# Kernel tuning notes

Hardware: AMD Instinct MI355X
Metric: run time of the kernel (lower is better)

## Reference

```python
import jax, jax.numpy as jnp
import numpy as np

D_K = 64
NEG_INF = -1.0e9


def setup_inputs() -> dict:
    key = jax.random.key(0)
    kq, kk, kv = jax.random.split(key, 3)
    B, H, S, D = 2, 16, 2048, D_K
    Q = jax.random.normal(kq, (B, H, S, D), dtype=jnp.float32)
    K = jax.random.normal(kk, (B, H, S, D), dtype=jnp.float32)
    V = jax.random.normal(kv, (B, H, S, D), dtype=jnp.float32)
    # causal mask: True where attention is DISALLOWED (strict upper triangle)
    attn_mask = jnp.triu(jnp.ones((S, S), dtype=bool), k=1)
    return {"Q": Q, "K": K, "V": V, "attn_mask": attn_mask}


def reference(Q, K, V, attn_mask):
    # scores = Q @ (K / sqrt(d_k))^T  -> [B,H,S,S]
    scale = 1.0 / np.sqrt(D_K).astype(np.float32)
    scores = jnp.einsum("bhqd,bhkd->bhqk", Q, K * scale)
    scores = jnp.where(attn_mask, NEG_INF, scores)  # masked_fill_(mask, -1e9)
    attn = jax.nn.softmax(scores, axis=-1)
    context = jnp.einsum("bhqk,bhkd->bhqd", attn, V)
    return (context, attn)
```

## Files before the change

### kernel.cpp

```cpp
#include <hip/hip_runtime.h>

constexpr int S_LEN = 2048;
constexpr int D_K   = 64;
constexpr int N_BH  = 32;
constexpr int KB    = 64;

typedef __attribute__((ext_vector_type(8))) short short8;
typedef __attribute__((ext_vector_type(4))) float f32x4;
typedef unsigned short ushort_t;

__device__ __forceinline__ unsigned short f2bf(float f) {
    unsigned int u = __builtin_bit_cast(unsigned int, f);
    u += 0x7fffu + ((u >> 16) & 1u);
    return (unsigned short)(u >> 16);
}
__device__ __forceinline__ float bf2f(unsigned short h) {
    unsigned int u = ((unsigned int)h) << 16;
    return __builtin_bit_cast(float, u);
}

__global__ __launch_bounds__(256)
void prep_k(const float* __restrict__ K, ushort_t* __restrict__ Kws) {
    const int idx = blockIdx.x * 256 + threadIdx.x;
    const float4* src = (const float4*)K + (size_t)idx * 2;
    float4 a = src[0], b = src[1];
    float x[8] = {a.x, a.y, a.z, a.w, b.x, b.y, b.z, b.w};
    short8 o;
    #pragma unroll
    for (int j = 0; j < 8; ++j) o[j] = (short)f2bf(x[j] * 0.125f);
    *(short8*)(Kws + (size_t)idx * 8) = o;
}

__global__ __launch_bounds__(256)
void prep_v(const float* __restrict__ V, ushort_t* __restrict__ Vws) {
    const int gid = blockIdx.x * 256 + threadIdx.x;
    const int u   = gid & 511;
    const int bc  = gid >> 9;
    const int c   = bc & 31;
    const int bh  = bc >> 5;
    const int kg  = u >> 6;
    const int d   = u & 63;
    const float* vp = V + ((size_t)bh * S_LEN + c * KB + kg * 8) * D_K + d;
    short8 o;
    #pragma unroll
    for (int i = 0; i < 8; ++i) o[i] = (short)f2bf(vp[(size_t)i * D_K]);
    *(short8*)(Vws + ((size_t)(bh * 32 + c) * D_K + d) * KB + kg * 8) = o;
}

__global__ __launch_bounds__(256, 4)
void sdpa_main(const float* __restrict__ Q, const ushort_t* __restrict__ Kws,
               const ushort_t* __restrict__ Vws, float* __restrict__ out)
{
    __shared__ __align__(16) ushort_t Kbuf[2][4096];
    __shared__ __align__(16) ushort_t Vbuf[2][4096];
    __shared__ __align__(16) ushort_t Plds[4][1024];

    const int tid = threadIdx.x;
    const int w   = tid >> 6;
    const int l   = tid & 63;
    const int lr  = l & 15;
    const int lh  = l >> 4;

    const int bx  = blockIdx.x;
    const int g   = bx >> 8;
    const int idx = bx & 255;
    const int bh  = idx >> 3;
    const int r   = idx & 7;
    int t;
    switch (g) {
        case 0:  t = r;      break;
        case 1:  t = 15 - r; break;
        case 2:  t = 16 + r; break;
        default: t = 31 - r; break;
    }
    const int nch = t + 1;
    const int q0  = t * 64;
    const int qg_base = q0 + w * 16 + lh * 4;

    float* ctx_out  = out;
    float* attn_out = out + (size_t)N_BH * S_LEN * D_K;

    const short8* Kt  = (const short8*)(Kws + (size_t)bh * S_LEN * D_K);
    const short8* Vt8 = (const short8*)(Vws + (size_t)bh * 32 * 4096);

    const int wrow0  = tid >> 3;
    const int wcol   = (tid & 7) << 4;
    const int wphys0 = wrow0 * 128 + (wcol ^ ((wrow0 & 7) << 4));
    const int wphys1 = wphys0 + 32 * 128;
    const int rsw    = (lr & 7) << 4;

    short8 qhi[2], qlo[2];
    {
        const float* qrow = Q + ((size_t)bh * S_LEN + q0 + w * 16 + lr) * D_K;
        #pragma unroll
        for (int ds = 0; ds < 2; ++ds) {
            const float4* p4 = (const float4*)(qrow + ds * 32 + lh * 8);
            float4 a = p4[0], bq = p4[1];
            float x[8] = {a.x, a.y, a.z, a.w, bq.x, bq.y, bq.z, bq.w};
            short8 hi, lo;
            #pragma unroll
            for (int j = 0; j < 8; ++j) {
                unsigned short h = f2bf(x[j]);
                hi[j] = (short)h;
                lo[j] = (short)f2bf(x[j] - bf2f(h));
            }
            qhi[ds] = hi; qlo[ds] = lo;
        }
    }

    float inv_[4];
    {
        float sum[4] = {0.f, 0.f, 0.f, 0.f};

        auto p1 = [&](const char* Kb, int c) {
            #pragma unroll
            for (int nt = 0; nt < 4; ++nt) {
                f32x4 acc = {0.f, 0.f, 0.f, 0.f};
                #pragma unroll
                for (int ks = 0; ks < 2; ++ks) {
                    short8 bk = *(const short8*)(Kb + (nt * 16 + lr) * 128 + ((ks * 64 + lh * 16) ^ rsw));
                    acc = __builtin_amdgcn_mfma_f32_16x16x32_bf16(qhi[ks], bk, acc, 0, 0, 0);
                }
                const int kg = c * KB + nt * 16 + lr;
                #pragma unroll
                for (int rr = 0; rr < 4; ++rr)
                    if (kg <= qg_base + rr) sum[rr] += __expf(fminf(acc[rr], 60.f));
            }
        };

        short8 kE0 = Kt[tid], kE1 = Kt[tid + 256];
        *(short8*)((char*)&Kbuf[0][0] + wphys0) = kE0;
        *(short8*)((char*)&Kbuf[0][0] + wphys1) = kE1;
        short8 kO0 = Kt[512 + tid], kO1 = Kt[512 + tid + 256];
        __syncthreads();
        for (int c = 0; c < nch; c += 2) {
            if (c + 2 < nch) { kE0 = Kt[(c + 2) * 512 + tid]; kE1 = Kt[(c + 2) * 512 + tid + 256]; }
            p1((const char*)&Kbuf[0][0], c);
            if (c + 1 < nch) {
                *(short8*)((char*)&Kbuf[1][0] + wphys0) = kO0;
                *(short8*)((char*)&Kbuf[1][0] + wphys1) = kO1;
            }
            __syncthreads();
            if (c + 1 < nch) {
                if (c + 3 < nch) { kO0 = Kt[(c + 3) * 512 + tid]; kO1 = Kt[(c + 3) * 512 + tid + 256]; }
                p1((const char*)&Kbuf[1][0], c + 1);
                if (c + 2 < nch) {
                    *(short8*)((char*)&Kbuf[0][0] + wphys0) = kE0;
                    *(short8*)((char*)&Kbuf[0][0] + wphys1) = kE1;
                }
                __syncthreads();
            }
        }
        #pragma unroll
        for (int rr = 0; rr < 4; ++rr) {
            float s = sum[rr];
            s += __shfl_xor(s, 1);
            s += __shfl_xor(s, 2);
            s += __shfl_xor(s, 4);
            s += __shfl_xor(s, 8);
            inv_[rr] = 1.f / s;
        }
    }

    f32x4 ctx[4];
    #pragma unroll
    for (int nt = 0; nt < 4; ++nt) ctx[nt] = (f32x4){0.f, 0.f, 0.f, 0.f};

    {
        auto p2 = [&](const char* Kb, const char* Vb, int c) {
            #pragma unroll
            for (int nt = 0; nt < 4; ++nt) {
                f32x4 acc = {0.f, 0.f, 0.f, 0.f};
                #pragma unroll
                for (int ks = 0; ks < 2; ++ks) {
                    short8 bk = *(const short8*)(Kb + (nt * 16 + lr) * 128 + ((ks * 64 + lh * 16) ^ rsw));
                    acc = __builtin_amdgcn_mfma_f32_16x16x32_bf16(qhi[ks], bk, acc, 0, 0, 0);
                    acc = __builtin_amdgcn_mfma_f32_16x16x32_bf16(qlo[ks], bk, acc, 0, 0, 0);
                }
                const int kg = c * KB + nt * 16 + lr;
                #pragma unroll
                for (int rr = 0; rr < 4; ++rr) {
                    const int pwr = lh * 4 + rr;
                    const int qg  = qg_base + rr;
                    float p = (kg <= qg) ? __expf(fminf(acc[rr], 60.f)) * inv_[rr] : 0.f;
                    attn_out[((size_t)bh * S_LEN + qg) * S_LEN + kg] = p;
                    Plds[w][pwr * 64 + ((nt * 16 + lr) ^ ((pwr & 7) << 3))] = f2bf(p);
                }
            }
            #pragma unroll
            for (int ks = 0; ks < 2; ++ks) {
                short8 pa = *(const short8*)&Plds[w][lr * 64 + ((ks * 32 + lh * 8) ^ ((lr & 7) << 3))];
                #pragma unroll
                for (int nt = 0; nt < 4; ++nt) {
                    short8 vb = *(const short8*)(Vb + (nt * 16 + lr) * 128 + ((ks * 64 + lh * 16) ^ rsw));
                    ctx[nt] = __builtin_amdgcn_mfma_f32_16x16x32_bf16(pa, vb, ctx[nt], 0, 0, 0);
                }
            }
        };

        short8 kE0 = Kt[tid],        kE1 = Kt[tid + 256];
        short8 vE0 = Vt8[tid],       vE1 = Vt8[tid + 256];
        *(short8*)((char*)&Kbuf[0][0] + wphys0) = kE0;
        *(short8*)((char*)&Kbuf[0][0] + wphys1) = kE1;
        *(short8*)((char*)&Vbuf[0][0] + wphys0) = vE0;
        *(short8*)((char*)&Vbuf[0][0] + wphys1) = vE1;
        short8 kO0 = Kt[512 + tid],  kO1 = Kt[512 + tid + 256];
        short8 vO0 = Vt8[512 + tid], vO1 = Vt8[512 + tid + 256];
        __syncthreads();
        for (int c = 0; c < nch; c += 2) {
            if (c + 2 < nch) {
                kE0 = Kt[(c + 2) * 512 + tid];  kE1 = Kt[(c + 2) * 512 + tid + 256];
                vE0 = Vt8[(c + 2) * 512 + tid]; vE1 = Vt8[(c + 2) * 512 + tid + 256];
            }
            p2((const char*)&Kbuf[0][0], (const char*)&Vbuf[0][0], c);
            if (c + 1 < nch) {
                *(short8*)((char*)&Kbuf[1][0] + wphys0) = kO0;
                *(short8*)((char*)&Kbuf[1][0] + wphys1) = kO1;
                *(short8*)((char*)&Vbuf[1][0] + wphys0) = vO0;
                *(short8*)((char*)&Vbuf[1][0] + wphys1) = vO1;
            }
            __syncthreads();
            if (c + 1 < nch) {
                if (c + 3 < nch) {
                    kO0 = Kt[(c + 3) * 512 + tid];  kO1 = Kt[(c + 3) * 512 + tid + 256];
                    vO0 = Vt8[(c + 3) * 512 + tid]; vO1 = Vt8[(c + 3) * 512 + tid + 256];
                }
                p2((const char*)&Kbuf[1][0], (const char*)&Vbuf[1][0], c + 1);
                if (c + 2 < nch) {
                    *(short8*)((char*)&Kbuf[0][0] + wphys0) = kE0;
                    *(short8*)((char*)&Kbuf[0][0] + wphys1) = kE1;
                    *(short8*)((char*)&Vbuf[0][0] + wphys0) = vE0;
                    *(short8*)((char*)&Vbuf[0][0] + wphys1) = vE1;
                }
                __syncthreads();
            }
        }
    }

    #pragma unroll
    for (int nt = 0; nt < 4; ++nt)
        #pragma unroll
        for (int rr = 0; rr < 4; ++rr)
            ctx_out[((size_t)bh * S_LEN + qg_base + rr) * D_K + nt * 16 + lr] = ctx[nt][rr];

    const int k0 = nch * KB;
    if (k0 < S_LEN) {
        const float4 z = {0.f, 0.f, 0.f, 0.f};
        float* rowp = attn_out + ((size_t)bh * S_LEN + q0 + (tid >> 2)) * S_LEN;
        for (int k = k0 + (tid & 3) * 4; k < S_LEN; k += 16)
            *(float4*)(rowp + k) = z;
    }
}

constexpr int LDP = 72;

__global__ __launch_bounds__(256)
void sdpa_fused_v1(const float* __restrict__ Q, const float* __restrict__ K,
                   const float* __restrict__ V, float* __restrict__ out)
{
    __shared__ __align__(16) unsigned short Klds[KB * LDP];
    __shared__ __align__(16) unsigned short Vtlds[D_K * LDP];
    __shared__ __align__(16) unsigned short Pl[4][16 * LDP];

    const int tid = threadIdx.x;
    const int w   = tid >> 6;
    const int l   = tid & 63;
    const int lr  = l & 15;
    const int lh  = l >> 4;

    const int bh   = blockIdx.y;
    const int qblk = (int)gridDim.x - 1 - (int)blockIdx.x;
    const int q0   = qblk * 64;
    const int qw   = q0 + w * 16;
    const int nchunks = qblk + 1;

    const size_t in_base = (size_t)bh * S_LEN * D_K;
    float* ctx_out  = out;
    float* attn_out = out + (size_t)N_BH * S_LEN * D_K;

    short8 qhi[2], qlo[2];
    {
        const float* qrow = Q + in_base + (size_t)(qw + lr) * D_K;
        #pragma unroll
        for (int ds = 0; ds < 2; ++ds) {
            const float4* p4 = (const float4*)(qrow + ds * 32 + lh * 8);
            float4 a = p4[0], b = p4[1];
            float x[8] = {a.x, a.y, a.z, a.w, b.x, b.y, b.z, b.w};
            short8 hi, lo;
            #pragma unroll
            for (int j = 0; j < 8; ++j) {
                unsigned short h = f2bf(x[j]);
                hi[j] = (short)h;
                lo[j] = (short)f2bf(x[j] - bf2f(h));
            }
            qhi[ds] = hi; qlo[ds] = lo;
        }
    }

    const int srow = tid >> 2;
    const int scol = (tid & 3) * 16;
    const float* kstage = K + in_base + (size_t)srow * D_K + scol;
    const float* vstage = V + in_base + (size_t)srow * D_K + scol;

    float inv_[4];
    {
        float sum[4] = {0.f, 0.f, 0.f, 0.f};
        for (int c = 0; c < nchunks; ++c) {
            {
                const float4* kp = (const float4*)(kstage + (size_t)c * KB * D_K);
                float4 a0 = kp[0], a1 = kp[1], a2 = kp[2], a3 = kp[3];
                float x[16] = {a0.x,a0.y,a0.z,a0.w, a1.x,a1.y,a1.z,a1.w,
                               a2.x,a2.y,a2.z,a2.w, a3.x,a3.y,a3.z,a3.w};
                short8 w0, w1;
                #pragma unroll
                for (int j = 0; j < 8; ++j) {
                    w0[j] = (short)f2bf(x[j]     * 0.125f);
                    w1[j] = (short)f2bf(x[j + 8] * 0.125f);
                }
                *(short8*)&Klds[srow * LDP + scol]     = w0;
                *(short8*)&Klds[srow * LDP + scol + 8] = w1;
            }
            __syncthreads();
            #pragma unroll
            for (int nt = 0; nt < 4; ++nt) {
                f32x4 acc = {0.f, 0.f, 0.f, 0.f};
                #pragma unroll
                for (int ks = 0; ks < 2; ++ks) {
                    short8 bk = *(const short8*)&Klds[(nt*16 + lr) * LDP + ks*32 + lh*8];
                    acc = __builtin_amdgcn_mfma_f32_16x16x32_bf16(qhi[ks], bk, acc, 0, 0, 0);
                    acc = __builtin_amdgcn_mfma_f32_16x16x32_bf16(qlo[ks], bk, acc, 0, 0, 0);
                }
                const int kg = c * KB + nt * 16 + lr;
                #pragma unroll
                for (int rr = 0; rr < 4; ++rr) {
                    if (kg <= qw + lh * 4 + rr)
                        sum[rr] += __expf(fminf(acc[rr], 60.f));
                }
            }
            __syncthreads();
        }
        #pragma unroll
        for (int rr = 0; rr < 4; ++rr) {
            float t = sum[rr];
            t += __shfl_xor(t, 1);
            t += __shfl_xor(t, 2);
            t += __shfl_xor(t, 4);
            t += __shfl_xor(t, 8);
            inv_[rr] = 1.f / t;
        }
    }

    f32x4 ctx[4];
    #pragma unroll
    for (int nt = 0; nt < 4; ++nt) ctx[nt] = (f32x4){0.f, 0.f, 0.f, 0.f};

    for (int c = 0; c < nchunks; ++c) {
        {
            const float4* kp = (const float4*)(kstage + (size_t)c * KB * D_K);
            float4 a0 = kp[0], a1 = kp[1], a2 = kp[2], a3 = kp[3];
            float x[16] = {a0.x,a0.y,a0.z,a0.w, a1.x,a1.y,a1.z,a1.w,
                           a2.x,a2.y,a2.z,a2.w, a3.x,a3.y,a3.z,a3.w};
            short8 w0, w1;
            #pragma unroll
            for (int j = 0; j < 8; ++j) {
                w0[j] = (short)f2bf(x[j]     * 0.125f);
                w1[j] = (short)f2bf(x[j + 8] * 0.125f);
            }
            *(short8*)&Klds[srow * LDP + scol]     = w0;
            *(short8*)&Klds[srow * LDP + scol + 8] = w1;

            const float4* vp = (const float4*)(vstage + (size_t)c * KB * D_K);
            float4 b0 = vp[0], b1 = vp[1], b2 = vp[2], b3 = vp[3];
            float y[16] = {b0.x,b0.y,b0.z,b0.w, b1.x,b1.y,b1.z,b1.w,
                           b2.x,b2.y,b2.z,b2.w, b3.x,b3.y,b3.z,b3.w};
            #pragma unroll
            for (int j = 0; j < 16; ++j)
                Vtlds[(scol + j) * LDP + srow] = f2bf(y[j]);
        }
        __syncthreads();

        #pragma unroll
        for (int nt = 0; nt < 4; ++nt) {
            f32x4 acc = {0.f, 0.f, 0.f, 0.f};
            #pragma unroll
            for (int ks = 0; ks < 2; ++ks) {
                short8 bk = *(const short8*)&Klds[(nt*16 + lr) * LDP + ks*32 + lh*8];
                acc = __builtin_amdgcn_mfma_f32_16x16x32_bf16(qhi[ks], bk, acc, 0, 0, 0);
                acc = __builtin_amdgcn_mfma_f32_16x16x32_bf16(qlo[ks], bk, acc, 0, 0, 0);
            }
            const int kg = c * KB + nt * 16 + lr;
            #pragma unroll
            for (int rr = 0; rr < 4; ++rr) {
                const int qg = qw + lh * 4 + rr;
                float p = (kg <= qg) ? __expf(fminf(acc[rr], 60.f)) * inv_[rr] : 0.f;
                attn_out[((size_t)bh * S_LEN + qg) * S_LEN + kg] = p;
                Pl[w][(lh * 4 + rr) * LDP + nt * 16 + lr] = f2bf(p);
            }
        }
        __syncthreads();

        #pragma unroll
        for (int ks = 0; ks < 2; ++ks) {
            short8 pa = *(const short8*)&Pl[w][lr * LDP + ks*32 + lh*8];
            #pragma unroll
            for (int nt = 0; nt < 4; ++nt) {
                short8 vb = *(const short8*)&Vtlds[(nt*16 + lr) * LDP + ks*32 + lh*8];
                ctx[nt] = __builtin_amdgcn_mfma_f32_16x16x32_bf16(pa, vb, ctx[nt], 0, 0, 0);
            }
        }
        __syncthreads();
    }

    #pragma unroll
    for (int nt = 0; nt < 4; ++nt)
        #pragma unroll
        for (int rr = 0; rr < 4; ++rr)
            ctx_out[((size_t)bh * S_LEN + qw + lh * 4 + rr) * D_K + nt * 16 + lr] = ctx[nt][rr];

    const int k0 = nchunks * KB;
    if (k0 < S_LEN) {
        const float4 z = {0.f, 0.f, 0.f, 0.f};
        for (int rr = 0; rr < 64; ++rr) {
            float* rowp = attn_out + ((size_t)bh * S_LEN + q0 + rr) * S_LEN;
            for (int k = k0 + tid * 4; k < S_LEN; k += 256 * 4)
                *(float4*)(rowp + k) = z;
        }
    }
}

extern "C" void kernel_launch(void* const* d_in, const int* in_sizes, int n_in,
                              void* d_out, int out_size, void* d_ws, size_t ws_size,
                              hipStream_t stream)
{
    const float* Q = (const float*)d_in[0];
    const float* K = (const float*)d_in[1];
    const float* V = (const float*)d_in[2];
    float* out = (float*)d_out;

    const size_t ws_needed = (size_t)2 * N_BH * S_LEN * D_K * sizeof(ushort_t);
    if (ws_size >= ws_needed) {
        ushort_t* Kws = (ushort_t*)d_ws;
        ushort_t* Vws = Kws + (size_t)N_BH * S_LEN * D_K;
        prep_k<<<2048, 256, 0, stream>>>(K, Kws);
        prep_v<<<2048, 256, 0, stream>>>(V, Vws);
        sdpa_main<<<1024, 256, 0, stream>>>(Q, Kws, Vws, out);
    } else {
        dim3 grid(S_LEN / 64, N_BH);
        sdpa_fused_v1<<<grid, 256, 0, stream>>>(Q, K, V, out);
    }
}
```

Baseline: 173.4 us.

## Load K/V fragments directly from global memory and remap block-to-head order

Drops the shared-memory double-buffered K/V staging and its barriers. Each wave now loads its MFMA B fragments straight from global memory into registers, relying on L1/L2 because all four waves read the same chunk. It also reorders the block index so that consecutive blocks cover eight heads at the same query tile, which may improve L2 locality and balance. The cost is redundant global loads per wave and no explicit prefetch, so load latency is exposed within each chunk.

After: 260.8 us. 50.4% more time.

```diff
diff --git a/kernel.cpp b/kernel.cpp
--- a/kernel.cpp
+++ b/kernel.cpp
@@ -51,8 +51,6 @@
 void sdpa_main(const float* __restrict__ Q, const ushort_t* __restrict__ Kws,
                const ushort_t* __restrict__ Vws, float* __restrict__ out)
 {
-    __shared__ __align__(16) ushort_t Kbuf[2][4096];
-    __shared__ __align__(16) ushort_t Vbuf[2][4096];
     __shared__ __align__(16) ushort_t Plds[4][1024];
 
     const int tid = threadIdx.x;
@@ -61,17 +59,20 @@
     const int lr  = l & 15;
     const int lh  = l >> 4;
 
-    const int bx  = blockIdx.x;
-    const int g   = bx >> 8;
-    const int idx = bx & 255;
-    const int bh  = idx >> 3;
-    const int r   = idx & 7;
+    const int bx = blockIdx.x;
+    const int x  = bx & 7;
+    const int m  = bx >> 3;
+    const int hh = m & 3;
+    const int j  = m >> 2;
+    const int bh = hh * 8 + x;
+    const int j0 = j & 7;
+    const int ji = j >> 3;
     int t;
-    switch (g) {
-        case 0:  t = r;      break;
-        case 1:  t = 15 - r; break;
-        case 2:  t = 16 + r; break;
-        default: t = 31 - r; break;
+    switch (ji) {
+        case 0:  t = j0;      break;
+        case 1:  t = 15 - j0; break;
+        case 2:  t = 16 + j0; break;
+        default: t = 31 - j0; break;
     }
     const int nch = t + 1;
     const int q0  = t * 64;
@@ -80,14 +81,8 @@
     float* ctx_out  = out;
     float* attn_out = out + (size_t)N_BH * S_LEN * D_K;
 
-    const short8* Kt  = (const short8*)(Kws + (size_t)bh * S_LEN * D_K);
-    const short8* Vt8 = (const short8*)(Vws + (size_t)bh * 32 * 4096);
-
-    const int wrow0  = tid >> 3;
-    const int wcol   = (tid & 7) << 4;
-    const int wphys0 = wrow0 * 128 + (wcol ^ ((wrow0 & 7) << 4));
-    const int wphys1 = wphys0 + 32 * 128;
-    const int rsw    = (lr & 7) << 4;
+    const ushort_t* Kb = Kws + (size_t)bh * S_LEN * D_K;
+    const ushort_t* Vb = Vws + (size_t)bh * 32 * 4096;
 
     short8 qhi[2], qlo[2];
     {
@@ -96,59 +91,41 @@
         for (int ds = 0; ds < 2; ++ds) {
             const float4* p4 = (const float4*)(qrow + ds * 32 + lh * 8);
             float4 a = p4[0], bq = p4[1];
-            float x[8] = {a.x, a.y, a.z, a.w, bq.x, bq.y, bq.z, bq.w};
+            float xx[8] = {a.x, a.y, a.z, a.w, bq.x, bq.y, bq.z, bq.w};
             short8 hi, lo;
             #pragma unroll
-            for (int j = 0; j < 8; ++j) {
-                unsigned short h = f2bf(x[j]);
-                hi[j] = (short)h;
-                lo[j] = (short)f2bf(x[j] - bf2f(h));
+            for (int jj = 0; jj < 8; ++jj) {
+                unsigned short h = f2bf(xx[jj]);
+                hi[jj] = (short)h;
+                lo[jj] = (short)f2bf(xx[jj] - bf2f(h));
             }
             qhi[ds] = hi; qlo[ds] = lo;
         }
     }
+
+    const int fbase = lr * 64 + lh * 8;
 
     float inv_[4];
     {
         float sum[4] = {0.f, 0.f, 0.f, 0.f};
-
-        auto p1 = [&](const char* Kb, int c) {
+        for (int c = 0; c < nch; ++c) {
+            const ushort_t* kc = Kb + (size_t)c * 4096;
+            short8 bk[8];
+            #pragma unroll
+            for (int nt = 0; nt < 4; ++nt)
+                #pragma unroll
+                for (int ks = 0; ks < 2; ++ks)
+                    bk[nt * 2 + ks] = *(const short8*)(kc + fbase + nt * 1024 + ks * 32);
             #pragma unroll
             for (int nt = 0; nt < 4; ++nt) {
                 f32x4 acc = {0.f, 0.f, 0.f, 0.f};
                 #pragma unroll
-                for (int ks = 0; ks < 2; ++ks) {
-                    short8 bk = *(const short8*)(Kb + (nt * 16 + lr) * 128 + ((ks * 64 + lh * 16) ^ rsw));
-                    acc = __builtin_amdgcn_mfma_f32_16x16x32_bf16(qhi[ks], bk, acc, 0, 0, 0);
-                }
+                for (int ks = 0; ks < 2; ++ks)
+                    acc = __builtin_amdgcn_mfma_f32_16x16x32_bf16(qhi[ks], bk[nt * 2 + ks], acc, 0, 0, 0);
                 const int kg = c * KB + nt * 16 + lr;
                 #pragma unroll
                 for (int rr = 0; rr < 4; ++rr)
                     if (kg <= qg_base + rr) sum[rr] += __expf(fminf(acc[rr], 60.f));
-            }
-        };
-
-        short8 kE0 = Kt[tid], kE1 = Kt[tid + 256];
-        *(short8*)((char*)&Kbuf[0][0] + wphys0) = kE0;
-        *(short8*)((char*)&Kbuf[0][0] + wphys1) = kE1;
-        short8 kO0 = Kt[512 + tid], kO1 = Kt[512 + tid + 256];
-        __syncthreads();
-        for (int c = 0; c < nch; c += 2) {
-            if (c + 2 < nch) { kE0 = Kt[(c + 2) * 512 + tid]; kE1 = Kt[(c + 2) * 512 + tid + 256]; }
-            p1((const char*)&Kbuf[0][0], c);
-            if (c + 1 < nch) {
-                *(short8*)((char*)&Kbuf[1][0] + wphys0) = kO0;
-                *(short8*)((char*)&Kbuf[1][0] + wphys1) = kO1;
-            }
-            __syncthreads();
-            if (c + 1 < nch) {
-                if (c + 3 < nch) { kO0 = Kt[(c + 3) * 512 + tid]; kO1 = Kt[(c + 3) * 512 + tid + 256]; }
-                p1((const char*)&Kbuf[1][0], c + 1);
-                if (c + 2 < nch) {
-                    *(short8*)((char*)&Kbuf[0][0] + wphys0) = kE0;
-                    *(short8*)((char*)&Kbuf[0][0] + wphys1) = kE1;
-                }
-                __syncthreads();
             }
         }
         #pragma unroll
@@ -166,74 +143,49 @@
     #pragma unroll
     for (int nt = 0; nt < 4; ++nt) ctx[nt] = (f32x4){0.f, 0.f, 0.f, 0.f};
 
-    {
-        auto p2 = [&](const char* Kb, const char* Vb, int c) {
-            #pragma unroll
-            for (int nt = 0; nt < 4; ++nt) {
-                f32x4 acc = {0.f, 0.f, 0.f, 0.f};
-                #pragma unroll
-                for (int ks = 0; ks < 2; ++ks) {
-                    short8 bk = *(const short8*)(Kb + (nt * 16 + lr) * 128 + ((ks * 64 + lh * 16) ^ rsw));
-                    acc = __builtin_amdgcn_mfma_f32_16x16x32_bf16(qhi[ks], bk, acc, 0, 0, 0);
-                    acc = __builtin_amdgcn_mfma_f32_16x16x32_bf16(qlo[ks], bk, acc, 0, 0, 0);
-                }
-                const int kg = c * KB + nt * 16 + lr;
-                #pragma unroll
-                for (int rr = 0; rr < 4; ++rr) {
-                    const int pwr = lh * 4 + rr;
-                    const int qg  = qg_base + rr;
-                    float p = (kg <= qg) ? __expf(fminf(acc[rr], 60.f)) * inv_[rr] : 0.f;
-                    attn_out[((size_t)bh * S_LEN + qg) * S_LEN + kg] = p;
-                    Plds[w][pwr * 64 + ((nt * 16 + lr) ^ ((pwr & 7) << 3))] = f2bf(p);
-                }
-            }
+    for (int c = 0; c < nch; ++c) {
+        const ushort_t* kc = Kb + (size_t)c * 4096;
+        const ushort_t* vc = Vb + (size_t)c * 4096;
+
+        short8 bk[8];
+        #pragma unroll
+        for (int nt = 0; nt < 4; ++nt)
+            #pragma unroll
+            for (int ks = 0; ks < 2; ++ks)
+                bk[nt * 2 + ks] = *(const short8*)(kc + fbase + nt * 1024 + ks * 32);
+
+        #pragma unroll
+        for (int nt = 0; nt < 4; ++nt) {
+            f32x4 acc = {0.f, 0.f, 0.f, 0.f};
             #pragma unroll
             for (int ks = 0; ks < 2; ++ks) {
-                short8 pa = *(const short8*)&Plds[w][lr * 64 + ((ks * 32 + lh * 8) ^ ((lr & 7) << 3))];
-                #pragma unroll
-                for (int nt = 0; nt < 4; ++nt) {
-                    short8 vb = *(const short8*)(Vb + (nt * 16 + lr) * 128 + ((ks * 64 + lh * 16) ^ rsw));
-                    ctx[nt] = __builtin_amdgcn_mfma_f32_16x16x32_bf16(pa, vb, ctx[nt], 0, 0, 0);
-                }
-            }
-        };
-
-        short8 kE0 = Kt[tid],        kE1 = Kt[tid + 256];
-        short8 vE0 = Vt8[tid],       vE1 = Vt8[tid + 256];
-        *(short8*)((char*)&Kbuf[0][0] + wphys0) = kE0;
-        *(short8*)((char*)&Kbuf[0][0] + wphys1) = kE1;
-        *(short8*)((char*)&Vbuf[0][0] + wphys0) = vE0;
-        *(short8*)((char*)&Vbuf[0][0] + wphys1) = vE1;
-        short8 kO0 = Kt[512 + tid],  kO1 = Kt[512 + tid + 256];
-        short8 vO0 = Vt8[512 + tid], vO1 = Vt8[512 + tid + 256];
-        __syncthreads();
-        for (int c = 0; c < nch; c += 2) {
-            if (c + 2 < nch) {
-                kE0 = Kt[(c + 2) * 512 + tid];  kE1 = Kt[(c + 2) * 512 + tid + 256];
-                vE0 = Vt8[(c + 2) * 512 + tid]; vE1 = Vt8[(c + 2) * 512 + tid + 256];
-            }
-            p2((const char*)&Kbuf[0][0], (const char*)&Vbuf[0][0], c);
-            if (c + 1 < nch) {
-                *(short8*)((char*)&Kbuf[1][0] + wphys0) = kO0;
-                *(short8*)((char*)&Kbuf[1][0] + wphys1) = kO1;
-                *(short8*)((char*)&Vbuf[1][0] + wphys0) = vO0;
-                *(short8*)((char*)&Vbuf[1][0] + wphys1) = vO1;
-            }
-            __syncthreads();
-            if (c + 1 < nch) {
-                if (c + 3 < nch) {
-                    kO0 = Kt[(c + 3) * 512 + tid];  kO1 = Kt[(c + 3) * 512 + tid + 256];
-                    vO0 = Vt8[(c + 3) * 512 + tid]; vO1 = Vt8[(c + 3) * 512 + tid + 256];
-                }
-                p2((const char*)&Kbuf[1][0], (const char*)&Vbuf[1][0], c + 1);
-                if (c + 2 < nch) {
-                    *(short8*)((char*)&Kbuf[0][0] + wphys0) = kE0;
-                    *(short8*)((char*)&Kbuf[0][0] + wphys1) = kE1;
-                    *(short8*)((char*)&Vbuf[0][0] + wphys0) = vE0;
-                    *(short8*)((char*)&Vbuf[0][0] + wphys1) = vE1;
-                }
-                __syncthreads();
-            }
+                acc = __builtin_amdgcn_mfma_f32_16x16x32_bf16(qhi[ks], bk[nt * 2 + ks], acc, 0, 0, 0);
+                acc = __builtin_amdgcn_mfma_f32_16x16x32_bf16(qlo[ks], bk[nt * 2 + ks], acc, 0, 0, 0);
+            }
+            const int kg = c * KB + nt * 16 + lr;
+            #pragma unroll
+            for (int rr = 0; rr < 4; ++rr) {
+                const int pwr = lh * 4 + rr;
+                const int qg  = qg_base + rr;
+                float p = (kg <= qg) ? __expf(fminf(acc[rr], 60.f)) * inv_[rr] : 0.f;
+                attn_out[((size_t)bh * S_LEN + qg) * S_LEN + kg] = p;
+                Plds[w][pwr * 64 + ((nt * 16 + lr) ^ ((pwr & 7) << 3))] = f2bf(p);
+            }
+        }
+
+        short8 vb[8];
+        #pragma unroll
+        for (int nt = 0; nt < 4; ++nt)
+            #pragma unroll
+            for (int ks = 0; ks < 2; ++ks)
+                vb[nt * 2 + ks] = *(const short8*)(vc + fbase + nt * 1024 + ks * 32);
+
+        short8 pa0 = *(const short8*)&Plds[w][lr * 64 + ((lh * 8) ^ ((lr & 7) << 3))];
+        short8 pa1 = *(const short8*)&Plds[w][lr * 64 + ((32 + lh * 8) ^ ((lr & 7) << 3))];
+        #pragma unroll
+        for (int nt = 0; nt < 4; ++nt) {
+            ctx[nt] = __builtin_amdgcn_mfma_f32_16x16x32_bf16(pa0, vb[nt * 2 + 0], ctx[nt], 0, 0, 0);
+            ctx[nt] = __builtin_amdgcn_mfma_f32_16x16x32_bf16(pa1, vb[nt * 2 + 1], ctx[nt], 0, 0, 0);
         }
     }
 
```

## Halve attention block to 32 query rows, single-buffer LDS, nontemporal attn stores

Applied to the files above, without the earlier changes.

Each block of sdpa_main now has two waves covering 32 query rows instead of four waves covering 64, and the grid doubles to 2048 blocks. The aim is finer causal load balancing and more resident blocks per CU. The K/V LDS tiles become single-buffered with a register prefetch of the next chunk, which cuts LDS use but leaves less overlap between loads and compute. The large attention-probability output and its zero-fill are now written with nontemporal stores to reduce cache pollution on this bandwidth-bound write.

After: 229.6 us. 1.32x slower.

```diff
diff --git a/kernel.cpp b/kernel.cpp
--- a/kernel.cpp
+++ b/kernel.cpp
@@ -47,13 +47,13 @@
     *(short8*)(Vws + ((size_t)(bh * 32 + c) * D_K + d) * KB + kg * 8) = o;
 }
 
-__global__ __launch_bounds__(256, 4)
+__global__ __launch_bounds__(128, 4)
 void sdpa_main(const float* __restrict__ Q, const ushort_t* __restrict__ Kws,
                const ushort_t* __restrict__ Vws, float* __restrict__ out)
 {
-    __shared__ __align__(16) ushort_t Kbuf[2][4096];
-    __shared__ __align__(16) ushort_t Vbuf[2][4096];
-    __shared__ __align__(16) ushort_t Plds[4][1024];
+    __shared__ __align__(16) ushort_t Kbuf[4096];
+    __shared__ __align__(16) ushort_t Vbuf[4096];
+    __shared__ __align__(16) ushort_t Plds[2][1024];
 
     const int tid = threadIdx.x;
     const int w   = tid >> 6;
@@ -62,19 +62,19 @@
     const int lh  = l >> 4;
 
     const int bx  = blockIdx.x;
-    const int g   = bx >> 8;
-    const int idx = bx & 255;
-    const int bh  = idx >> 3;
-    const int r   = idx & 7;
+    const int g   = bx >> 9;
+    const int idx = bx & 511;
+    const int bh  = idx >> 4;
+    const int r   = idx & 15;
     int t;
     switch (g) {
         case 0:  t = r;      break;
-        case 1:  t = 15 - r; break;
-        case 2:  t = 16 + r; break;
-        default: t = 31 - r; break;
-    }
-    const int nch = t + 1;
-    const int q0  = t * 64;
+        case 1:  t = 31 - r; break;
+        case 2:  t = 32 + r; break;
+        default: t = 63 - r; break;
+    }
+    const int nch = (t >> 1) + 1;
+    const int q0  = t * 32;
     const int qg_base = q0 + w * 16 + lh * 4;
 
     float* ctx_out  = out;
@@ -86,7 +86,6 @@
     const int wrow0  = tid >> 3;
     const int wcol   = (tid & 7) << 4;
     const int wphys0 = wrow0 * 128 + (wcol ^ ((wrow0 & 7) << 4));
-    const int wphys1 = wphys0 + 32 * 128;
     const int rsw    = (lr & 7) << 4;
 
     short8 qhi[2], qlo[2];
@@ -112,7 +111,8 @@
     {
         float sum[4] = {0.f, 0.f, 0.f, 0.f};
 
-        auto p1 = [&](const char* Kb, int c) {
+        auto p1 = [&](int c) {
+            const char* Kb = (const char*)&Kbuf[0];
             #pragma unroll
             for (int nt = 0; nt < 4; ++nt) {
                 f32x4 acc = {0.f, 0.f, 0.f, 0.f};
@@ -128,26 +128,25 @@
             }
         };
 
-        short8 kE0 = Kt[tid], kE1 = Kt[tid + 256];
-        *(short8*)((char*)&Kbuf[0][0] + wphys0) = kE0;
-        *(short8*)((char*)&Kbuf[0][0] + wphys1) = kE1;
-        short8 kO0 = Kt[512 + tid], kO1 = Kt[512 + tid + 256];
+        short8 kn0 = Kt[tid],       kn1 = Kt[tid + 128];
+        short8 kn2 = Kt[tid + 256], kn3 = Kt[tid + 384];
+        *(short8*)((char*)&Kbuf[0] + wphys0)        = kn0;
+        *(short8*)((char*)&Kbuf[0] + wphys0 + 2048) = kn1;
+        *(short8*)((char*)&Kbuf[0] + wphys0 + 4096) = kn2;
+        *(short8*)((char*)&Kbuf[0] + wphys0 + 6144) = kn3;
         __syncthreads();
-        for (int c = 0; c < nch; c += 2) {
-            if (c + 2 < nch) { kE0 = Kt[(c + 2) * 512 + tid]; kE1 = Kt[(c + 2) * 512 + tid + 256]; }
-            p1((const char*)&Kbuf[0][0], c);
+        for (int c = 0; c < nch; ++c) {
             if (c + 1 < nch) {
-                *(short8*)((char*)&Kbuf[1][0] + wphys0) = kO0;
-                *(short8*)((char*)&Kbuf[1][0] + wphys1) = kO1;
-            }
+                const int b0 = (c + 1) * 512 + tid;
+                kn0 = Kt[b0]; kn1 = Kt[b0 + 128]; kn2 = Kt[b0 + 256]; kn3 = Kt[b0 + 384];
+            }
+            p1(c);
             __syncthreads();
             if (c + 1 < nch) {
-                if (c + 3 < nch) { kO0 = Kt[(c + 3) * 512 + tid]; kO1 = Kt[(c + 3) * 512 + tid + 256]; }
-                p1((const char*)&Kbuf[1][0], c + 1);
-                if (c + 2 < nch) {
-                    *(short8*)((char*)&Kbuf[0][0] + wphys0) = kE0;
-                    *(short8*)((char*)&Kbuf[0][0] + wphys1) = kE1;
-                }
+                *(short8*)((char*)&Kbuf[0] + wphys0)        = kn0;
+                *(short8*)((char*)&Kbuf[0] + wphys0 + 2048) = kn1;
+                *(short8*)((char*)&Kbuf[0] + wphys0 + 4096) = kn2;
+                *(short8*)((char*)&Kbuf[0] + wphys0 + 6144) = kn3;
                 __syncthreads();
             }
         }
@@ -167,7 +166,9 @@
     for (int nt = 0; nt < 4; ++nt) ctx[nt] = (f32x4){0.f, 0.f, 0.f, 0.f};
 
     {
-        auto p2 = [&](const char* Kb, const char* Vb, int c) {
+        auto p2 = [&](int c) {
+            const char* Kb = (const char*)&Kbuf[0];
+            const char* Vb = (const char*)&Vbuf[0];
             #pragma unroll
             for (int nt = 0; nt < 4; ++nt) {
                 f32x4 acc = {0.f, 0.f, 0.f, 0.f};
@@ -183,7 +184,7 @@
                     const int pwr = lh * 4 + rr;
                     const int qg  = qg_base + rr;
                     float p = (kg <= qg) ? __expf(fminf(acc[rr], 60.f)) * inv_[rr] : 0.f;
-                    attn_out[((size_t)bh * S_LEN + qg) * S_LEN + kg] = p;
+                    __builtin_nontemporal_store(p, attn_out + ((size_t)bh * S_LEN + qg) * S_LEN + kg);
                     Plds[w][pwr * 64 + ((nt * 16 + lr) ^ ((pwr & 7) << 3))] = f2bf(p);
                 }
             }
@@ -198,40 +199,36 @@
             }
         };
 
-        short8 kE0 = Kt[tid],        kE1 = Kt[tid + 256];
-        short8 vE0 = Vt8[tid],       vE1 = Vt8[tid + 256];
-        *(short8*)((char*)&Kbuf[0][0] + wphys0) = kE0;
-        *(short8*)((char*)&Kbuf[0][0] + wphys1) = kE1;
-        *(short8*)((char*)&Vbuf[0][0] + wphys0) = vE0;
-        *(short8*)((char*)&Vbuf[0][0] + wphys1) = vE1;
-        short8 kO0 = Kt[512 + tid],  kO1 = Kt[512 + tid + 256];
-        short8 vO0 = Vt8[512 + tid], vO1 = Vt8[512 + tid + 256];
+        short8 kn0 = Kt[tid],        kn1 = Kt[tid + 128];
+        short8 kn2 = Kt[tid + 256],  kn3 = Kt[tid + 384];
+        short8 vn0 = Vt8[tid],       vn1 = Vt8[tid + 128];
+        short8 vn2 = Vt8[tid + 256], vn3 = Vt8[tid + 384];
+        *(short8*)((char*)&Kbuf[0] + wphys0)        = kn0;
+        *(short8*)((char*)&Kbuf[0] + wphys0 + 2048) = kn1;
+        *(short8*)((char*)&Kbuf[0] + wphys0 + 4096) = kn2;
+        *(short8*)((char*)&Kbuf[0] + wphys0 + 6144) = kn3;
+        *(short8*)((char*)&Vbuf[0] + wphys0)        = vn0;
+        *(short8*)((char*)&Vbuf[0] + wphys0 + 2048) = vn1;
+        *(short8*)((char*)&Vbuf[0] + wphys0 + 4096) = vn2;
+        *(short8*)((char*)&Vbuf[0] + wphys0 + 6144) = vn3;
         __syncthreads();
-        for (int c = 0; c < nch; c += 2) {
-            if (c + 2 < nch) {
-                kE0 = Kt[(c + 2) * 512 + tid];  kE1 = Kt[(c + 2) * 512 + tid + 256];
-                vE0 = Vt8[(c + 2) * 512 + tid]; vE1 = Vt8[(c + 2) * 512 + tid + 256];
-            }
-            p2((const char*)&Kbuf[0][0], (const char*)&Vbuf[0][0], c);
+        for (int c = 0; c < nch; ++c) {
             if (c + 1 < nch) {
-                *(short8*)((char*)&Kbuf[1][0] + wphys0) = kO0;
-                *(short8*)((char*)&Kbuf[1][0] + wphys1) = kO1;
-                *(short8*)((char*)&Vbuf[1][0] + wphys0) = vO0;
-                *(short8*)((char*)&Vbuf[1][0] + wphys1) = vO1;
-            }
+                const int b0 = (c + 1) * 512 + tid;
+                kn0 = Kt[b0];  kn1 = Kt[b0 + 128];  kn2 = Kt[b0 + 256];  kn3 = Kt[b0 + 384];
+                vn0 = Vt8[b0]; vn1 = Vt8[b0 + 128]; vn2 = Vt8[b0 + 256]; vn3 = Vt8[b0 + 384];
+            }
+            p2(c);
             __syncthreads();
             if (c + 1 < nch) {
-                if (c + 3 < nch) {
-                    kO0 = Kt[(c + 3) * 512 + tid];  kO1 = Kt[(c + 3) * 512 + tid + 256];
-                    vO0 = Vt8[(c + 3) * 512 + tid]; vO1 = Vt8[(c + 3) * 512 + tid + 256];
-                }
-                p2((const char*)&Kbuf[1][0], (const char*)&Vbuf[1][0], c + 1);
-                if (c + 2 < nch) {
-                    *(short8*)((char*)&Kbuf[0][0] + wphys0) = kE0;
-                    *(short8*)((char*)&Kbuf[0][0] + wphys1) = kE1;
-                    *(short8*)((char*)&Vbuf[0][0] + wphys0) = vE0;
-                    *(short8*)((char*)&Vbuf[0][0] + wphys1) = vE1;
-                }
+                *(short8*)((char*)&Kbuf[0] + wphys0)        = kn0;
+                *(short8*)((char*)&Kbuf[0] + wphys0 + 2048) = kn1;
+                *(short8*)((char*)&Kbuf[0] + wphys0 + 4096) = kn2;
+                *(short8*)((char*)&Kbuf[0] + wphys0 + 6144) = kn3;
+                *(short8*)((char*)&Vbuf[0] + wphys0)        = vn0;
+                *(short8*)((char*)&Vbuf[0] + wphys0 + 2048) = vn1;
+                *(short8*)((char*)&Vbuf[0] + wphys0 + 4096) = vn2;
+                *(short8*)((char*)&Vbuf[0] + wphys0 + 6144) = vn3;
                 __syncthreads();
             }
         }
@@ -245,10 +242,10 @@
 
     const int k0 = nch * KB;
     if (k0 < S_LEN) {
-        const float4 z = {0.f, 0.f, 0.f, 0.f};
+        const f32x4 z = {0.f, 0.f, 0.f, 0.f};
         float* rowp = attn_out + ((size_t)bh * S_LEN + q0 + (tid >> 2)) * S_LEN;
         for (int k = k0 + (tid & 3) * 4; k < S_LEN; k += 16)
-            *(float4*)(rowp + k) = z;
+            __builtin_nontemporal_store(z, (f32x4*)(rowp + k));
     }
 }
 
@@ -443,7 +440,7 @@
         ushort_t* Vws = Kws + (size_t)N_BH * S_LEN * D_K;
         prep_k<<<2048, 256, 0, stream>>>(K, Kws);
         prep_v<<<2048, 256, 0, stream>>>(V, Vws);
-        sdpa_main<<<1024, 256, 0, stream>>>(Q, Kws, Vws, out);
+        sdpa_main<<<2048, 128, 0, stream>>>(Q, Kws, Vws, out);
     } else {
         dim3 grid(S_LEN / 64, N_BH);
         sdpa_fused_v1<<<grid, 256, 0, stream>>>(Q, K, V, out);
```
